# Kernel optimization log

Measured on AMD Instinct MI355X. Metric: run time of the kernel, lower is better.

## Reference

```python
import jax, jax.numpy as jnp
import numpy as np
from jax import lax

C_IN, C_KEY, C_VAL = 1024, 256, 512

def conv3x3(x, w, b):
    # x: [B,C_in,H,W], w: [C_out,C_in,3,3] -> SAME padding, stride 1
    y = lax.conv_general_dilated(x, w, window_strides=(1, 1), padding='SAME',
                                 dimension_numbers=('NCHW', 'OIHW', 'NCHW'))
    return y + b[None, :, None, None]

def setup_inputs() -> dict:
    key = jax.random.key(0)
    ks = jax.random.split(key, 10)
    B, H, W = 16, 32, 32
    conv_std = 0.01  # matches torch init.normal_(std=0.01)
    inp = {
        'src_temp': jax.random.normal(ks[0], (B, C_IN, H, W), jnp.float32),
        'src_search': jax.random.normal(ks[1], (B, C_IN, H, W), jnp.float32),
        'wk_m': jax.random.normal(ks[2], (C_KEY, C_IN, 3, 3), jnp.float32) * conv_std,
        'bk_m': jnp.zeros((C_KEY,), jnp.float32),
        'wv_m': jax.random.normal(ks[3], (C_VAL, C_IN, 3, 3), jnp.float32) * conv_std,
        'bv_m': jnp.zeros((C_VAL,), jnp.float32),
        'wk_q': jax.random.normal(ks[4], (C_KEY, C_IN, 3, 3), jnp.float32) * conv_std,
        'bk_q': jnp.zeros((C_KEY,), jnp.float32),
        'wv_q': jax.random.normal(ks[5], (C_VAL, C_IN, 3, 3), jnp.float32) * conv_std,
        'bv_q': jnp.zeros((C_VAL,), jnp.float32),
    }
    return inp

def reference(src_temp, src_search, wk_m, bk_m, wv_m, bv_m, wk_q, bk_q, wv_q, bv_q):
    # key/value projections
    m_key = conv3x3(src_temp, wk_m, bk_m)      # [B, Ck, H, W]
    m_value = conv3x3(src_temp, wv_m, bv_m)    # [B, Cv, H, W]
    q_key = conv3x3(src_search, wk_q, bk_q)    # [B, Ck, H, W]
    q_value = conv3x3(src_search, wv_q, bv_q)  # [B, Cv, H, W]

    B, Ck, H, W = m_key.shape
    Cv = m_value.shape[1]
    HW = H * W

    mk = m_key.reshape(B, Ck, HW)   # [B, Ck, HW_m]
    qk = q_key.reshape(B, Ck, HW)   # [B, Ck, HW_q]
    # scores: [B, HW_m, HW_q]
    w = jnp.einsum('bcm,bcq->bmq', mk, qk) / jnp.sqrt(jnp.float32(Ck))
    w = jax.nn.softmax(w, axis=1)   # normalize over memory locations

    mv = m_value.reshape(B, Cv, HW)            # [B, Cv, HW_m]
    mem_info = jnp.einsum('bcm,bmq->bcq', mv, w).reshape(B, Cv, H, W)
    return jnp.concatenate([mem_info, q_value], axis=1)  # [B, 2*Cv, H, W]
```

## Files before the change

### kernel.cpp

```cpp
#include <hip/hip_runtime.h>
#include <stdint.h>

typedef __bf16 bf16;
typedef __bf16 bf16x8 __attribute__((ext_vector_type(8)));
typedef float  f32x4  __attribute__((ext_vector_type(4)));
typedef unsigned int u32;

#define OFF_AHI   0ull
#define OFF_ALO   18939904ull
#define OFF_WHI   37879808ull
#define OFF_WLO   52035584ull
#define OFF_QKEYT 67108864ull
#define OFF_MKEYT 83886080ull
#define OFF_MVAL  100663296ull
#define OFF_WATTN 0ull

__device__ __forceinline__ void split(float v, bf16& h, bf16& l) {
    h = (bf16)v;
    l = (bf16)(v - (float)h);
}

__device__ __forceinline__ u32 packsplit(float v) {
    bf16 h = (bf16)v;
    bf16 l = (bf16)(v - (float)h);
    unsigned short hu = __builtin_bit_cast(unsigned short, h);
    unsigned short lu = __builtin_bit_cast(unsigned short, l);
    return (u32)hu | ((u32)lu << 16);
}

__device__ __forceinline__ void deint4(const uint4 v, uint2& h, uint2& l) {
    h.x = (v.x & 0xffffu) | (v.y << 16);
    h.y = (v.z & 0xffffu) | (v.w << 16);
    l.x = (v.x >> 16) | (v.y & 0xffff0000u);
    l.y = (v.z >> 16) | (v.w & 0xffff0000u);
}

__global__ __launch_bounds__(256) void k_wt(const float* __restrict__ wk,
                                            const float* __restrict__ wv,
                                            bf16* __restrict__ Wh, bf16* __restrict__ Wl) {
    size_t id = (size_t)blockIdx.x * 256 + threadIdx.x;
    int e = (int)(id & 7);
    size_t t = id >> 3;
    int mm = (int)(t % 96); t /= 96;
    int coff = (int)(t & 3); t >>= 2;
    int cch = (int)(t & 31); t >>= 5;
    int r = (int)(t % 9);
    int mt = (int)(t / 9);
    int m = mt * 96 + mm;
    int c = cch * 32 + coff * 8 + e;
    float v = (m < 256) ? wk[((size_t)m * 1024 + c) * 9 + r]
                        : wv[((size_t)(m - 256) * 1024 + c) * 9 + r];
    bf16 h, l;
    split(v, h, l);
    Wh[id] = h; Wl[id] = l;
}

__global__ __launch_bounds__(256) void k_zero(bf16* __restrict__ Ah, bf16* __restrict__ Al) {
    int id = blockIdx.x * 256 + threadIdx.x;
    int oct = id & 127;
    int t = id >> 7;
    int pos = t % 132; t /= 132;
    int bl = t & 7, hl = t >> 3;
    int yy, xx;
    if (pos < 34)       { yy = 0;  xx = pos; }
    else if (pos < 68)  { yy = 33; xx = pos - 34; }
    else if (pos < 100) { yy = pos - 68 + 1;  xx = 0; }
    else                { yy = pos - 100 + 1; xx = 33; }
    bf16* base = hl ? Al : Ah;
    size_t off = (((size_t)bl * 34 + yy) * 34 + xx) * 1024 + (size_t)oct * 8;
    *(uint4*)(base + off) = make_uint4(0u, 0u, 0u, 0u);
}

__global__ __launch_bounds__(256) void k_transpose(const float* __restrict__ src,
                                                   bf16* __restrict__ Ah, bf16* __restrict__ Al) {
    int pt = blockIdx.x, ct = blockIdx.y, bl = blockIdx.z;
    __shared__ float tile[64][68];
    int t = threadIdx.x;
    #pragma unroll
    for (int k = 0; k < 4; ++k) {
        int idx = t + 256 * k;
        int c = idx >> 4, f4 = idx & 15;
        float4 v = *(const float4*)(src + ((size_t)bl * 1024 + ct * 64 + c) * 1024 + pt * 64 + f4 * 4);
        *(float4*)&tile[c][f4 * 4] = v;
    }
    __syncthreads();
    #pragma unroll
    for (int k = 0; k < 2; ++k) {
        int s = t + 256 * k;
        int px = s >> 3, oct = s & 7;
        bf16x8 vh, vl;
        #pragma unroll
        for (int e = 0; e < 8; ++e) {
            bf16 h, l;
            split(tile[oct * 8 + e][px], h, l);
            vh[e] = h; vl[e] = l;
        }
        int pxg = pt * 64 + px;
        int yy = (pxg >> 5) + 1, xx = (pxg & 31) + 1;
        size_t off = (((size_t)bl * 34 + yy) * 34 + xx) * 1024 + ct * 64 + oct * 8;
        *(bf16x8*)(Ah + off) = vh;
        *(bf16x8*)(Al + off) = vl;
    }
}

#define XS_STRIDE 40
#define XS_HALF4  (4 * 34 * XS_STRIDE)
__global__ __launch_bounds__(256) void k_conv(const bf16* __restrict__ Ah, const bf16* __restrict__ Al,
                                              const bf16* __restrict__ Wh, const bf16* __restrict__ Wl,
                                              const float* __restrict__ biask, const float* __restrict__ biasv,
                                              u32* __restrict__ keyT, float* __restrict__ valf,
                                              u32* __restrict__ valp, int bglob) {
    int bl = blockIdx.x >> 4, rg = blockIdx.x & 15;
    int mt = blockIdx.y;
    int y0 = rg * 2;
    int b = bglob + bl;

    __shared__ bf16 Xs[2 * XS_HALF4];

    int tid = threadIdx.x;
    int w = tid >> 6, l = tid & 63;
    int wm = (w & 1) * 48, wn = (w >> 1) * 32;
    int lm = l & 15, lq = l >> 4;
    int koff = lq * 8;

    f32x4 acc[3][2] = {};

    const size_t Abase = ((size_t)bl * 34 + y0) * 34 * 1024;
    const size_t wlane = (size_t)lq * 768 + (size_t)lm * 8;

    for (int cch = 0; cch < 32; ++cch) {
        int c0 = cch * 32;
        bf16x8 xv[5];
        int lidx[5];
        #pragma unroll
        for (int it = 0; it < 5; ++it) {
            int s = tid + 256 * it;
            if (s < 1088) {
                int hl = s >= 544;
                int r544 = s - hl * 544;
                int row = r544 / 136;
                int rr = r544 - row * 136;
                int px = rr >> 2, oct = rr & 3;
                const bf16* base = hl ? Al : Ah;
                xv[it] = *(const bf16x8*)(base + Abase + ((size_t)row * 34 + px) * 1024 + c0 + oct * 8);
                lidx[it] = ((hl * 4 + row) * 34 + px) * XS_STRIDE + oct * 8;
            } else lidx[it] = -1;
        }
        __syncthreads();
        #pragma unroll
        for (int it = 0; it < 5; ++it)
            if (lidx[it] >= 0) *(bf16x8*)&Xs[lidx[it]] = xv[it];
        __syncthreads();

        #pragma unroll
        for (int r = 0; r < 9; ++r) {
            int dy = r / 3, dx = r % 3;
            size_t wblk = (((size_t)mt * 9 + r) * 32 + cch) * 3072 + wlane;
            bf16x8 ah[3], al[3];
            #pragma unroll
            for (int i = 0; i < 3; ++i) {
                size_t o = wblk + (size_t)(wm + i * 16) * 8;
                ah[i] = *(const bf16x8*)(Wh + o);
                al[i] = *(const bf16x8*)(Wl + o);
            }
            #pragma unroll
            for (int j = 0; j < 2; ++j) {
                int n = wn + j * 16 + lm;
                int lbase = (((n >> 5) + dy) * 34 + (n & 31) + dx) * XS_STRIDE + koff;
                bf16x8 bh  = *(const bf16x8*)&Xs[lbase];
                bf16x8 blo = *(const bf16x8*)&Xs[XS_HALF4 + lbase];
                #pragma unroll
                for (int i = 0; i < 3; ++i) {
                    acc[i][j] = __builtin_amdgcn_mfma_f32_16x16x32_bf16(ah[i], bh,  acc[i][j], 0, 0, 0);
                    acc[i][j] = __builtin_amdgcn_mfma_f32_16x16x32_bf16(ah[i], blo, acc[i][j], 0, 0, 0);
                    acc[i][j] = __builtin_amdgcn_mfma_f32_16x16x32_bf16(al[i], bh,  acc[i][j], 0, 0, 0);
                }
            }
        }
    }

    int col = lm, rowb = lq * 4;
    #pragma unroll
    for (int i = 0; i < 3; ++i) {
        int ch4 = mt * 96 + wm + i * 16 + rowb;
        #pragma unroll
        for (int j = 0; j < 2; ++j) {
            int px = rg * 64 + wn + j * 16 + col;
            if (ch4 < 256) {
                u32 p0 = packsplit(acc[i][j][0] + biask[ch4 + 0]);
                u32 p1 = packsplit(acc[i][j][1] + biask[ch4 + 1]);
                u32 p2 = packsplit(acc[i][j][2] + biask[ch4 + 2]);
                u32 p3 = packsplit(acc[i][j][3] + biask[ch4 + 3]);
                *(uint4*)(keyT + ((size_t)b * 1024 + px) * 256 + ch4) = make_uint4(p0, p1, p2, p3);
            } else {
                int cv = ch4 - 256;
                if (valp) {
                    #pragma unroll
                    for (int e = 0; e < 4; ++e)
                        valp[((size_t)b * 512 + cv + e) * 1024 + px] = packsplit(acc[i][j][e] + biasv[cv + e]);
                } else {
                    #pragma unroll
                    for (int e = 0; e < 4; ++e)
                        valf[((size_t)b * 1024 + 512 + cv + e) * 1024 + px] = acc[i][j][e] + biasv[cv + e];
                }
            }
        }
    }
}

#define AS 40
__global__ __launch_bounds__(256) void k_scores(const u32* __restrict__ qkT,
                                                const u32* __restrict__ mkT,
                                                float* __restrict__ wattn) {
    int mt = blockIdx.x, qt = blockIdx.y, b = blockIdx.z;
    __shared__ bf16 Qh[128][AS], Ql[128][AS], Mh[128][AS], Ml[128][AS];
    int t = threadIdx.x;
    int w_ = t >> 6, l = t & 63;
    int wq = (w_ & 1) * 64, wm = (w_ >> 1) * 64;
    int lm = l & 15, lq = l >> 4, koff = lq * 8;
    int srow = t >> 1, sc4 = (t & 1) * 16;
    const u32* qbase = qkT + ((size_t)b * 1024 + qt * 128 + srow) * 256 + sc4;
    const u32* mbase = mkT + ((size_t)b * 1024 + mt * 128 + srow) * 256 + sc4;
    f32x4 acc[4][4] = {};
    uint4 qv[4], mv[4];
    #pragma unroll
    for (int k = 0; k < 4; ++k) { qv[k] = *(const uint4*)(qbase + k * 4); mv[k] = *(const uint4*)(mbase + k * 4); }
    for (int cc = 0; cc < 8; ++cc) {
        __syncthreads();
        #pragma unroll
        for (int k = 0; k < 4; ++k) {
            uint2 h, lo;
            deint4(qv[k], h, lo);
            *(uint2*)&Qh[srow][sc4 + k * 4] = h;
            *(uint2*)&Ql[srow][sc4 + k * 4] = lo;
            deint4(mv[k], h, lo);
            *(uint2*)&Mh[srow][sc4 + k * 4] = h;
            *(uint2*)&Ml[srow][sc4 + k * 4] = lo;
        }
        __syncthreads();
        if (cc < 7) {
            #pragma unroll
            for (int k = 0; k < 4; ++k) {
                qv[k] = *(const uint4*)(qbase + (cc + 1) * 32 + k * 4);
                mv[k] = *(const uint4*)(mbase + (cc + 1) * 32 + k * 4);
            }
        }
        bf16x8 ah[4], al[4];
        #pragma unroll
        for (int iq = 0; iq < 4; ++iq) {
            ah[iq] = *(const bf16x8*)&Qh[wq + iq * 16 + lm][koff];
            al[iq] = *(const bf16x8*)&Ql[wq + iq * 16 + lm][koff];
        }
        #pragma unroll
        for (int jm = 0; jm < 4; ++jm) {
            bf16x8 bh = *(const bf16x8*)&Mh[wm + jm * 16 + lm][koff];
            bf16x8 bl = *(const bf16x8*)&Ml[wm + jm * 16 + lm][koff];
            #pragma unroll
            for (int iq = 0; iq < 4; ++iq) {
                acc[iq][jm] = __builtin_amdgcn_mfma_f32_16x16x32_bf16(ah[iq], bh, acc[iq][jm], 0, 0, 0);
                acc[iq][jm] = __builtin_amdgcn_mfma_f32_16x16x32_bf16(ah[iq], bl, acc[iq][jm], 0, 0, 0);
                acc[iq][jm] = __builtin_amdgcn_mfma_f32_16x16x32_bf16(al[iq], bh, acc[iq][jm], 0, 0, 0);
            }
        }
    }
    #pragma unroll
    for (int iq = 0; iq < 4; ++iq) {
        int q = qt * 128 + wq + iq * 16 + lq * 4;
        #pragma unroll
        for (int jm = 0; jm < 4; ++jm) {
            int m = mt * 128 + wm + jm * 16 + lm;
            float* wp = wattn + ((size_t)b * 1024 + q) * 1024 + m;
            #pragma unroll
            for (int e = 0; e < 4; ++e)
                wp[(size_t)e * 1024] = acc[iq][jm][e] * 0.0625f;
        }
    }
}

__global__ __launch_bounds__(256) void k_softmax(float* __restrict__ wattn) {
    int row = blockIdx.x * 4 + (threadIdx.x >> 6);
    int l = threadIdx.x & 63;
    float* base = wattn + (size_t)row * 1024;
    float4 v[4];
    #pragma unroll
    for (int k = 0; k < 4; ++k) v[k] = *(float4*)(base + l * 4 + k * 256);
    float f[16];
    #pragma unroll
    for (int k = 0; k < 4; ++k) { f[4*k]=v[k].x; f[4*k+1]=v[k].y; f[4*k+2]=v[k].z; f[4*k+3]=v[k].w; }
    float mx = -3.0e38f;
    #pragma unroll
    for (int e = 0; e < 16; ++e) mx = fmaxf(mx, f[e]);
    #pragma unroll
    for (int off = 32; off > 0; off >>= 1) mx = fmaxf(mx, __shfl_xor(mx, off));
    float s = 0.0f;
    #pragma unroll
    for (int e = 0; e < 16; ++e) { f[e] = __expf(f[e] - mx); s += f[e]; }
    #pragma unroll
    for (int off = 32; off > 0; off >>= 1) s += __shfl_xor(s, off);
    float inv = 1.0f / s;
    u32* ub = (u32*)base;
    #pragma unroll
    for (int k = 0; k < 4; ++k) {
        uint4 u = make_uint4(packsplit(f[4*k]   * inv), packsplit(f[4*k+1] * inv),
                             packsplit(f[4*k+2] * inv), packsplit(f[4*k+3] * inv));
        *(uint4*)(ub + l * 4 + k * 256) = u;
    }
}

__global__ __launch_bounds__(256) void k_memv(const u32* __restrict__ mvalp,
                                              const u32* __restrict__ wattnp,
                                              float* __restrict__ outp) {
    int ct = blockIdx.x, qt = blockIdx.y, b = blockIdx.z;
    __shared__ bf16 Vh[128][AS], Vl[128][AS], Wh[128][AS], Wl[128][AS];
    int t = threadIdx.x;
    int w_ = t >> 6, l = t & 63;
    int wc = (w_ & 1) * 64, wq = (w_ >> 1) * 64;
    int lm = l & 15, lq = l >> 4, koff = lq * 8;
    int srow = t >> 1, sc4 = (t & 1) * 16;
    const u32* vbase = mvalp  + ((size_t)b * 512  + ct * 128 + srow) * 1024 + sc4;
    const u32* wbase = wattnp + ((size_t)b * 1024 + qt * 128 + srow) * 1024 + sc4;
    f32x4 acc[4][4] = {};
    uint4 vv[4], wv[4];
    #pragma unroll
    for (int k = 0; k < 4; ++k) { vv[k] = *(const uint4*)(vbase + k * 4); wv[k] = *(const uint4*)(wbase + k * 4); }
    for (int mc = 0; mc < 32; ++mc) {
        __syncthreads();
        #pragma unroll
        for (int k = 0; k < 4; ++k) {
            uint2 h, lo;
            deint4(vv[k], h, lo);
            *(uint2*)&Vh[srow][sc4 + k * 4] = h;
            *(uint2*)&Vl[srow][sc4 + k * 4] = lo;
            deint4(wv[k], h, lo);
            *(uint2*)&Wh[srow][sc4 + k * 4] = h;
            *(uint2*)&Wl[srow][sc4 + k * 4] = lo;
        }
        __syncthreads();
        if (mc < 31) {
            #pragma unroll
            for (int k = 0; k < 4; ++k) {
                vv[k] = *(const uint4*)(vbase + (mc + 1) * 32 + k * 4);
                wv[k] = *(const uint4*)(wbase + (mc + 1) * 32 + k * 4);
            }
        }
        bf16x8 ah[4], al[4];
        #pragma unroll
        for (int ic = 0; ic < 4; ++ic) {
            ah[ic] = *(const bf16x8*)&Vh[wc + ic * 16 + lm][koff];
            al[ic] = *(const bf16x8*)&Vl[wc + ic * 16 + lm][koff];
        }
        #pragma unroll
        for (int jq = 0; jq < 4; ++jq) {
            bf16x8 bh = *(const bf16x8*)&Wh[wq + jq * 16 + lm][koff];
            bf16x8 bl = *(const bf16x8*)&Wl[wq + jq * 16 + lm][koff];
            #pragma unroll
            for (int ic = 0; ic < 4; ++ic) {
                acc[ic][jq] = __builtin_amdgcn_mfma_f32_16x16x32_bf16(ah[ic], bh, acc[ic][jq], 0, 0, 0);
                acc[ic][jq] = __builtin_amdgcn_mfma_f32_16x16x32_bf16(ah[ic], bl, acc[ic][jq], 0, 0, 0);
                acc[ic][jq] = __builtin_amdgcn_mfma_f32_16x16x32_bf16(al[ic], bh, acc[ic][jq], 0, 0, 0);
            }
        }
    }
    #pragma unroll
    for (int ic = 0; ic < 4; ++ic) {
        int c = ct * 128 + wc + ic * 16 + lq * 4;
        #pragma unroll
        for (int jq = 0; jq < 4; ++jq) {
            int q = qt * 128 + wq + jq * 16 + lm;
            #pragma unroll
            for (int e = 0; e < 4; ++e)
                outp[((size_t)b * 1024 + c + e) * 1024 + q] = acc[ic][jq][e];
        }
    }
}

extern "C" void kernel_launch(void* const* d_in, const int* in_sizes, int n_in,
                              void* d_out, int out_size, void* d_ws, size_t ws_size,
                              hipStream_t stream) {
    const float* src_temp   = (const float*)d_in[0];
    const float* src_search = (const float*)d_in[1];
    const float* wk_m = (const float*)d_in[2];
    const float* bk_m = (const float*)d_in[3];
    const float* wv_m = (const float*)d_in[4];
    const float* bv_m = (const float*)d_in[5];
    const float* wk_q = (const float*)d_in[6];
    const float* bk_q = (const float*)d_in[7];
    const float* wv_q = (const float*)d_in[8];
    const float* bv_q = (const float*)d_in[9];
    float* out = (float*)d_out;
    char* ws = (char*)d_ws;
    bf16* Ah = (bf16*)(ws + OFF_AHI);
    bf16* Al = (bf16*)(ws + OFF_ALO);
    bf16* Wh = (bf16*)(ws + OFF_WHI);
    bf16* Wl = (bf16*)(ws + OFF_WLO);
    u32* qkP = (u32*)(ws + OFF_QKEYT);
    u32* mkP = (u32*)(ws + OFF_MKEYT);
    u32* mvP = (u32*)(ws + OFF_MVAL);
    float* wattn = (float*)(ws + OFF_WATTN);
    u32* wattnP = (u32*)(ws + OFF_WATTN);

    hipLaunchKernelGGL(k_zero, dim3(1056), dim3(256), 0, stream, Ah, Al);

    hipLaunchKernelGGL(k_wt, dim3(27648), dim3(256), 0, stream, wk_q, wv_q, Wh, Wl);
    for (int h = 0; h < 2; ++h) {
        hipLaunchKernelGGL(k_transpose, dim3(16, 16, 8), dim3(256), 0, stream,
                           src_search + (size_t)h * 8 * 1024 * 1024, Ah, Al);
        hipLaunchKernelGGL(k_conv, dim3(128, 8), dim3(256), 0, stream,
                           Ah, Al, Wh, Wl, bk_q, bv_q, qkP, out, (u32*)nullptr, h * 8);
    }
    hipLaunchKernelGGL(k_wt, dim3(27648), dim3(256), 0, stream, wk_m, wv_m, Wh, Wl);
    for (int h = 0; h < 2; ++h) {
        hipLaunchKernelGGL(k_transpose, dim3(16, 16, 8), dim3(256), 0, stream,
                           src_temp + (size_t)h * 8 * 1024 * 1024, Ah, Al);
        hipLaunchKernelGGL(k_conv, dim3(128, 8), dim3(256), 0, stream,
                           Ah, Al, Wh, Wl, bk_m, bv_m, mkP, (float*)nullptr, mvP, h * 8);
    }

    hipLaunchKernelGGL(k_scores,  dim3(8, 8, 16), dim3(256), 0, stream, qkP, mkP, wattn);
    hipLaunchKernelGGL(k_softmax, dim3(4096),     dim3(256), 0, stream, wattn);
    hipLaunchKernelGGL(k_memv,    dim3(4, 8, 16), dim3(256), 0, stream, mvP, wattnP, out);
}
```

Measured before the change: 1.601 ms.

## Run the search conv over all 16 batches with 4-row tiles and reordered grid

```diff
diff --git a/kernel.cpp b/kernel.cpp
--- a/kernel.cpp
+++ b/kernel.cpp
@@ -6,13 +6,17 @@
 typedef float  f32x4  __attribute__((ext_vector_type(4)));
 typedef unsigned int u32;
 
-#define OFF_AHI   0ull
-#define OFF_ALO   18939904ull
-#define OFF_WHI   37879808ull
-#define OFF_WLO   52035584ull
-#define OFF_QKEYT 67108864ull
-#define OFF_MKEYT 83886080ull
-#define OFF_MVAL  100663296ull
+#define OFF_A16HI 0ull
+#define OFF_A16LO 37879808ull
+#define OFF_A8HI  0ull
+#define OFF_A8LO  18939904ull
+#define OFF_W1HI  75759616ull
+#define OFF_W1LO  89915392ull
+#define OFF_W0HI  37879808ull
+#define OFF_W0LO  52035584ull
+#define OFF_MKEYT 67108864ull
+#define OFF_MVAL  83886080ull
+#define OFF_QKEYT 117440512ull
 #define OFF_WATTN 0ull
 
 __device__ __forceinline__ void split(float v, bf16& h, bf16& l) {
@@ -55,20 +59,18 @@
     Wh[id] = h; Wl[id] = l;
 }
 
-__global__ __launch_bounds__(256) void k_zero(bf16* __restrict__ Ah, bf16* __restrict__ Al) {
+__global__ __launch_bounds__(256) void k_zero(bf16* __restrict__ A) {
     int id = blockIdx.x * 256 + threadIdx.x;
     int oct = id & 127;
     int t = id >> 7;
     int pos = t % 132; t /= 132;
-    int bl = t & 7, hl = t >> 3;
     int yy, xx;
     if (pos < 34)       { yy = 0;  xx = pos; }
     else if (pos < 68)  { yy = 33; xx = pos - 34; }
     else if (pos < 100) { yy = pos - 68 + 1;  xx = 0; }
     else                { yy = pos - 100 + 1; xx = 33; }
-    bf16* base = hl ? Al : Ah;
-    size_t off = (((size_t)bl * 34 + yy) * 34 + xx) * 1024 + (size_t)oct * 8;
-    *(uint4*)(base + off) = make_uint4(0u, 0u, 0u, 0u);
+    size_t off = (((size_t)t * 1156) + yy * 34 + xx) * 1024 + (size_t)oct * 8;
+    *(uint4*)(A + off) = make_uint4(0u, 0u, 0u, 0u);
 }
 
 __global__ __launch_bounds__(256) void k_transpose(const float* __restrict__ src,
@@ -104,18 +106,126 @@
 }
 
 #define XS_STRIDE 40
-#define XS_HALF4  (4 * 34 * XS_STRIDE)
-__global__ __launch_bounds__(256) void k_conv(const bf16* __restrict__ Ah, const bf16* __restrict__ Al,
-                                              const bf16* __restrict__ Wh, const bf16* __restrict__ Wl,
-                                              const float* __restrict__ biask, const float* __restrict__ biasv,
-                                              u32* __restrict__ keyT, float* __restrict__ valf,
-                                              u32* __restrict__ valp, int bglob) {
-    int bl = blockIdx.x >> 4, rg = blockIdx.x & 15;
-    int mt = blockIdx.y;
+
+#define XS_H6 (6 * 34 * XS_STRIDE)
+__global__ __launch_bounds__(256) void k_conv16(const bf16* __restrict__ Ah, const bf16* __restrict__ Al,
+                                                const bf16* __restrict__ Wh, const bf16* __restrict__ Wl,
+                                                const float* __restrict__ biask, const float* __restrict__ biasv,
+                                                u32* __restrict__ keyT, float* __restrict__ valf) {
+    int id = blockIdx.x;
+    int mt = id & 7;
+    int r2 = id >> 3;
+    int bl = r2 >> 3;
+    int rg = r2 & 7;
+    int y0 = rg * 4;
+    int b = bl;
+
+    __shared__ bf16 Xs[2 * XS_H6];
+
+    int tid = threadIdx.x;
+    int w = tid >> 6, l = tid & 63;
+    int wm = (w & 1) * 48, wn = (w >> 1) * 64;
+    int lm = l & 15, lq = l >> 4;
+    int koff = lq * 8;
+
+    f32x4 acc[3][4] = {};
+
+    const size_t Abase = ((size_t)bl * 34 + y0) * 34 * 1024;
+    const size_t wlane = (size_t)lq * 768 + (size_t)lm * 8;
+
+    const bf16* gsrc[7];
+    int lidx[7];
+    #pragma unroll
+    for (int it = 0; it < 7; ++it) {
+        int s = tid + 256 * it;
+        if (s < 1632) {
+            int hl = s >= 816;
+            int r816 = s - hl * 816;
+            int row = r816 / 136;
+            int rr = r816 - row * 136;
+            int px = rr >> 2, oct = rr & 3;
+            const bf16* base = hl ? Al : Ah;
+            gsrc[it] = base + Abase + ((size_t)row * 34 + px) * 1024 + oct * 8;
+            lidx[it] = ((hl * 6 + row) * 34 + px) * XS_STRIDE + oct * 8;
+        } else { gsrc[it] = nullptr; lidx[it] = -1; }
+    }
+
+    for (int cch = 0; cch < 32; ++cch) {
+        int c0 = cch * 32;
+        bf16x8 xv[7];
+        #pragma unroll
+        for (int it = 0; it < 7; ++it)
+            if (lidx[it] >= 0) xv[it] = *(const bf16x8*)(gsrc[it] + c0);
+        __syncthreads();
+        #pragma unroll
+        for (int it = 0; it < 7; ++it)
+            if (lidx[it] >= 0) *(bf16x8*)&Xs[lidx[it]] = xv[it];
+        __syncthreads();
+
+        #pragma unroll
+        for (int r = 0; r < 9; ++r) {
+            int dy = r / 3, dx = r % 3;
+            size_t wblk = (((size_t)mt * 9 + r) * 32 + cch) * 3072 + wlane;
+            bf16x8 ah[3], al[3];
+            #pragma unroll
+            for (int i = 0; i < 3; ++i) {
+                size_t o = wblk + (size_t)(wm + i * 16) * 8;
+                ah[i] = *(const bf16x8*)(Wh + o);
+                al[i] = *(const bf16x8*)(Wl + o);
+            }
+            #pragma unroll
+            for (int j = 0; j < 4; ++j) {
+                int n = wn + j * 16 + lm;
+                int lbase = (((n >> 5) + dy) * 34 + (n & 31) + dx) * XS_STRIDE + koff;
+                bf16x8 bh  = *(const bf16x8*)&Xs[lbase];
+                bf16x8 blo = *(const bf16x8*)&Xs[XS_H6 + lbase];
+                #pragma unroll
+                for (int i = 0; i < 3; ++i) {
+                    acc[i][j] = __builtin_amdgcn_mfma_f32_16x16x32_bf16(ah[i], bh,  acc[i][j], 0, 0, 0);
+                    acc[i][j] = __builtin_amdgcn_mfma_f32_16x16x32_bf16(ah[i], blo, acc[i][j], 0, 0, 0);
+                    acc[i][j] = __builtin_amdgcn_mfma_f32_16x16x32_bf16(al[i], bh,  acc[i][j], 0, 0, 0);
+                }
+            }
+        }
+    }
+
+    int col = lm, rowb = lq * 4;
+    #pragma unroll
+    for (int i = 0; i < 3; ++i) {
+        int ch4 = mt * 96 + wm + i * 16 + rowb;
+        #pragma unroll
+        for (int j = 0; j < 4; ++j) {
+            int px = rg * 128 + wn + j * 16 + col;
+            if (ch4 < 256) {
+                u32 p0 = packsplit(acc[i][j][0] + biask[ch4 + 0]);
+                u32 p1 = packsplit(acc[i][j][1] + biask[ch4 + 1]);
+                u32 p2 = packsplit(acc[i][j][2] + biask[ch4 + 2]);
+                u32 p3 = packsplit(acc[i][j][3] + biask[ch4 + 3]);
+                *(uint4*)(keyT + ((size_t)b * 1024 + px) * 256 + ch4) = make_uint4(p0, p1, p2, p3);
+            } else {
+                int cv = ch4 - 256;
+                #pragma unroll
+                for (int e = 0; e < 4; ++e)
+                    valf[((size_t)b * 1024 + 512 + cv + e) * 1024 + px] = acc[i][j][e] + biasv[cv + e];
+            }
+        }
+    }
+}
+
+#define XS_H4 (4 * 34 * XS_STRIDE)
+__global__ __launch_bounds__(256) void k_conv8(const bf16* __restrict__ Ah, const bf16* __restrict__ Al,
+                                               const bf16* __restrict__ Wh, const bf16* __restrict__ Wl,
+                                               const float* __restrict__ biask, const float* __restrict__ biasv,
+                                               u32* __restrict__ keyT, u32* __restrict__ valp, int bglob) {
+    int id = blockIdx.x;
+    int mt = id & 7;
+    int r2 = id >> 3;
+    int bl = r2 >> 4;
+    int rg = r2 & 15;
     int y0 = rg * 2;
     int b = bglob + bl;
 
-    __shared__ bf16 Xs[2 * XS_HALF4];
+    __shared__ bf16 Xs[2 * XS_H4];
 
     int tid = threadIdx.x;
     int w = tid >> 6, l = tid & 63;
@@ -128,24 +238,29 @@
     const size_t Abase = ((size_t)bl * 34 + y0) * 34 * 1024;
     const size_t wlane = (size_t)lq * 768 + (size_t)lm * 8;
 
+    const bf16* gsrc[5];
+    int lidx[5];
+    #pragma unroll
+    for (int it = 0; it < 5; ++it) {
+        int s = tid + 256 * it;
+        if (s < 1088) {
+            int hl = s >= 544;
+            int r544 = s - hl * 544;
+            int row = r544 / 136;
+            int rr = r544 - row * 136;
+            int px = rr >> 2, oct = rr & 3;
+            const bf16* base = hl ? Al : Ah;
+            gsrc[it] = base + Abase + ((size_t)row * 34 + px) * 1024 + oct * 8;
+            lidx[it] = ((hl * 4 + row) * 34 + px) * XS_STRIDE + oct * 8;
+        } else { gsrc[it] = nullptr; lidx[it] = -1; }
+    }
+
     for (int cch = 0; cch < 32; ++cch) {
         int c0 = cch * 32;
         bf16x8 xv[5];
-        int lidx[5];
-        #pragma unroll
-        for (int it = 0; it < 5; ++it) {
-            int s = tid + 256 * it;
-            if (s < 1088) {
-                int hl = s >= 544;
-                int r544 = s - hl * 544;
-                int row = r544 / 136;
-                int rr = r544 - row * 136;
-                int px = rr >> 2, oct = rr & 3;
-                const bf16* base = hl ? Al : Ah;
-                xv[it] = *(const bf16x8*)(base + Abase + ((size_t)row * 34 + px) * 1024 + c0 + oct * 8);
-                lidx[it] = ((hl * 4 + row) * 34 + px) * XS_STRIDE + oct * 8;
-            } else lidx[it] = -1;
-        }
+        #pragma unroll
+        for (int it = 0; it < 5; ++it)
+            if (lidx[it] >= 0) xv[it] = *(const bf16x8*)(gsrc[it] + c0);
         __syncthreads();
         #pragma unroll
         for (int it = 0; it < 5; ++it)
@@ -168,7 +283,7 @@
                 int n = wn + j * 16 + lm;
                 int lbase = (((n >> 5) + dy) * 34 + (n & 31) + dx) * XS_STRIDE + koff;
                 bf16x8 bh  = *(const bf16x8*)&Xs[lbase];
-                bf16x8 blo = *(const bf16x8*)&Xs[XS_HALF4 + lbase];
+                bf16x8 blo = *(const bf16x8*)&Xs[XS_H4 + lbase];
                 #pragma unroll
                 for (int i = 0; i < 3; ++i) {
                     acc[i][j] = __builtin_amdgcn_mfma_f32_16x16x32_bf16(ah[i], bh,  acc[i][j], 0, 0, 0);
@@ -194,15 +309,9 @@
                 *(uint4*)(keyT + ((size_t)b * 1024 + px) * 256 + ch4) = make_uint4(p0, p1, p2, p3);
             } else {
                 int cv = ch4 - 256;
-                if (valp) {
-                    #pragma unroll
-                    for (int e = 0; e < 4; ++e)
-                        valp[((size_t)b * 512 + cv + e) * 1024 + px] = packsplit(acc[i][j][e] + biasv[cv + e]);
-                } else {
-                    #pragma unroll
-                    for (int e = 0; e < 4; ++e)
-                        valf[((size_t)b * 1024 + 512 + cv + e) * 1024 + px] = acc[i][j][e] + biasv[cv + e];
-                }
+                #pragma unroll
+                for (int e = 0; e < 4; ++e)
+                    valp[((size_t)b * 512 + cv + e) * 1024 + px] = packsplit(acc[i][j][e] + biasv[cv + e]);
             }
         }
     }
@@ -389,31 +498,36 @@
     const float* bv_q = (const float*)d_in[9];
     float* out = (float*)d_out;
     char* ws = (char*)d_ws;
-    bf16* Ah = (bf16*)(ws + OFF_AHI);
-    bf16* Al = (bf16*)(ws + OFF_ALO);
-    bf16* Wh = (bf16*)(ws + OFF_WHI);
-    bf16* Wl = (bf16*)(ws + OFF_WLO);
-    u32* qkP = (u32*)(ws + OFF_QKEYT);
-    u32* mkP = (u32*)(ws + OFF_MKEYT);
-    u32* mvP = (u32*)(ws + OFF_MVAL);
+
+    bf16* A    = (bf16*)(ws + OFF_A16HI);
+    bf16* Ah16 = (bf16*)(ws + OFF_A16HI);
+    bf16* Al16 = (bf16*)(ws + OFF_A16LO);
+    bf16* Ah8  = (bf16*)(ws + OFF_A8HI);
+    bf16* Al8  = (bf16*)(ws + OFF_A8LO);
+    bf16* W1h  = (bf16*)(ws + OFF_W1HI);
+    bf16* W1l  = (bf16*)(ws + OFF_W1LO);
+    bf16* W0h  = (bf16*)(ws + OFF_W0HI);
+    bf16* W0l  = (bf16*)(ws + OFF_W0LO);
+    u32* qkP   = (u32*)(ws + OFF_QKEYT);
+    u32* mkP   = (u32*)(ws + OFF_MKEYT);
+    u32* mvP   = (u32*)(ws + OFF_MVAL);
     float* wattn = (float*)(ws + OFF_WATTN);
-    u32* wattnP = (u32*)(ws + OFF_WATTN);
-
-    hipLaunchKernelGGL(k_zero, dim3(1056), dim3(256), 0, stream, Ah, Al);
-
-    hipLaunchKernelGGL(k_wt, dim3(27648), dim3(256), 0, stream, wk_q, wv_q, Wh, Wl);
+    u32* wattnP  = (u32*)(ws + OFF_WATTN);
+
+    hipLaunchKernelGGL(k_zero, dim3(2112), dim3(256), 0, stream, A);
+
+    hipLaunchKernelGGL(k_wt, dim3(27648), dim3(256), 0, stream, wk_q, wv_q, W1h, W1l);
+    hipLaunchKernelGGL(k_transpose, dim3(16, 16, 16), dim3(256), 0, stream,
+                       src_search, Ah16, Al16);
+    hipLaunchKernelGGL(k_conv16, dim3(1024), dim3(256), 0, stream,
+                       Ah16, Al16, W1h, W1l, bk_q, bv_q, qkP, out);
+
+    hipLaunchKernelGGL(k_wt, dim3(27648), dim3(256), 0, stream, wk_m, wv_m, W0h, W0l);
     for (int h = 0; h < 2; ++h) {
         hipLaunchKernelGGL(k_transpose, dim3(16, 16, 8), dim3(256), 0, stream,
-                           src_search + (size_t)h * 8 * 1024 * 1024, Ah, Al);
-        hipLaunchKernelGGL(k_conv, dim3(128, 8), dim3(256), 0, stream,
-                           Ah, Al, Wh, Wl, bk_q, bv_q, qkP, out, (u32*)nullptr, h * 8);
-    }
-    hipLaunchKernelGGL(k_wt, dim3(27648), dim3(256), 0, stream, wk_m, wv_m, Wh, Wl);
-    for (int h = 0; h < 2; ++h) {
-        hipLaunchKernelGGL(k_transpose, dim3(16, 16, 8), dim3(256), 0, stream,
-                           src_temp + (size_t)h * 8 * 1024 * 1024, Ah, Al);
-        hipLaunchKernelGGL(k_conv, dim3(128, 8), dim3(256), 0, stream,
-                           Ah, Al, Wh, Wl, bk_m, bv_m, mkP, (float*)nullptr, mvP, h * 8);
+                           src_temp + (size_t)h * 8 * 1024 * 1024, Ah8, Al8);
+        hipLaunchKernelGGL(k_conv8, dim3(1024), dim3(256), 0, stream,
+                           Ah8, Al8, W0h, W0l, bk_m, bv_m, mkP, mvP, h * 8);
     }
 
     hipLaunchKernelGGL(k_scores,  dim3(8, 8, 16), dim3(256), 0, stream, qkP, mkP, wattn);
```

Measured after the change: 1.636 ms. 2.2% more time.
